# Performance work log

Hardware: AMD Instinct MI355X
Metric: run time of the kernel (lower is better)

## Reference

```python
import jax, jax.numpy as jnp
import numpy as np

B, T, D, H, NL = 64, 1024, 64, 256, 2


def setup_inputs() -> dict:
    key = jax.random.key(0)
    ks = jax.random.split(key, 12)
    s_ih0 = 1.0 / np.sqrt(H)
    inp = {
        "x": jax.random.normal(ks[0], (B, T, D), dtype=jnp.float32),
        "W_ih0": jax.random.uniform(ks[1], (4 * H, D), jnp.float32, -s_ih0, s_ih0),
        "W_hh0": jax.random.uniform(ks[2], (4 * H, H), jnp.float32, -s_ih0, s_ih0),
        "b_ih0": jax.random.uniform(ks[3], (4 * H,), jnp.float32, -s_ih0, s_ih0),
        "b_hh0": jax.random.uniform(ks[4], (4 * H,), jnp.float32, -s_ih0, s_ih0),
        "W_ih1": jax.random.uniform(ks[5], (4 * H, H), jnp.float32, -s_ih0, s_ih0),
        "W_hh1": jax.random.uniform(ks[6], (4 * H, H), jnp.float32, -s_ih0, s_ih0),
        "b_ih1": jax.random.uniform(ks[7], (4 * H,), jnp.float32, -s_ih0, s_ih0),
        "b_hh1": jax.random.uniform(ks[8], (4 * H,), jnp.float32, -s_ih0, s_ih0),
        "fc_w": jax.random.uniform(ks[9], (1, H), jnp.float32, -s_ih0, s_ih0),
        "fc_b": jax.random.uniform(ks[10], (1,), jnp.float32, -s_ih0, s_ih0),
    }
    return inp


def _lstm_layer(x, W_ih, W_hh, b_ih, b_hh):
    # x: [B, T, Din] -> hidden sequence [B, T, H]
    h = W_hh.shape[1]
    # precompute input contribution for all timesteps (PyTorch gate order i,f,g,o)
    xg = jnp.einsum('btd,gd->btg', x, W_ih) + b_ih + b_hh  # [B, T, 4H]

    def step(carry, xt):
        hprev, cprev = carry
        gates = xt + hprev @ W_hh.T  # [B, 4H]
        i, f, g, o = jnp.split(gates, 4, axis=-1)
        i = jax.nn.sigmoid(i)
        f = jax.nn.sigmoid(f)
        g = jnp.tanh(g)
        o = jax.nn.sigmoid(o)
        c = f * cprev + i * g
        hnew = o * jnp.tanh(c)
        return (hnew, c), hnew

    b = x.shape[0]
    h0 = jnp.zeros((b, h), x.dtype)
    _, hs = jax.lax.scan(step, (h0, h0), jnp.swapaxes(xg, 0, 1))
    return jnp.swapaxes(hs, 0, 1)  # [B, T, H]


def reference(x, W_ih0, W_hh0, b_ih0, b_hh0, W_ih1, W_hh1, b_ih1, b_hh1, fc_w, fc_b):
    h1 = _lstm_layer(x, W_ih0, W_hh0, b_ih0, b_hh0)
    h2 = _lstm_layer(h1, W_ih1, W_hh1, b_ih1, b_hh1)
    last = h2[:, -1, :]  # [B, H]
    return last @ fc_w.T + fc_b  # [B, 1]
```

## Files before the change

kernel.cpp:

```cpp
#include <hip/hip_runtime.h>

#define B_ 64
#define TT 1024
#define HH 256

__device__ __forceinline__ float sigmoidf_(float x) { return 1.f / (1.f + __expf(-x)); }
__device__ __forceinline__ float fast_tanh(float x) {
    float e = __expf(2.f * x);
    return 1.f - 2.f / (e + 1.f);
}

__global__ __launch_bounds__(256) void xgemm_kernel(
    const float* __restrict__ A, const float* __restrict__ W,
    const float* __restrict__ bih, const float* __restrict__ bhh,
    float* __restrict__ out,
    int K, int RINGA, int s0A, int LC, int astr)
{
    __shared__ float As[16][132];
    __shared__ float Bs[16][132];
    const int tid = threadIdx.x;
    const int bm = (int)blockIdx.x >> 3;
    const int bn = (int)blockIdx.x & 7;
    const int m0 = bm << 7, n0 = bn << 7;
    const int ty = tid >> 4, tx = tid & 15;
    const int CM = (1 << LC) - 1;

    const float* arow[8];
    const float* brow[8];
#pragma unroll
    for (int i = 0; i < 8; ++i) {
        int mm = m0 + i * 16 + ty;
        int bb = mm >> LC, tc = mm & CM;
        int slot = s0A + tc; if (slot >= RINGA) slot -= RINGA;
        arow[i] = A + ((size_t)bb * RINGA + slot) * K * astr + tx * astr;
        brow[i] = W + (size_t)(n0 + i * 16 + ty) * K + tx;
    }

    float acc[8][8];
#pragma unroll
    for (int i = 0; i < 8; ++i)
#pragma unroll
        for (int j = 0; j < 8; ++j) acc[i][j] = 0.f;

    for (int kc = 0; kc < K; kc += 16) {
#pragma unroll
        for (int i = 0; i < 8; ++i) {
            As[tx][i * 16 + ty] = arow[i][kc * astr];
            Bs[tx][i * 16 + ty] = brow[i][kc];
        }
        __syncthreads();
#pragma unroll
        for (int k = 0; k < 16; ++k) {
            float a[8], bf[8];
#pragma unroll
            for (int j = 0; j < 8; ++j) a[j] = As[k][ty * 8 + j];
#pragma unroll
            for (int j = 0; j < 8; ++j) bf[j] = Bs[k][tx * 8 + j];
#pragma unroll
            for (int i = 0; i < 8; ++i)
#pragma unroll
                for (int j = 0; j < 8; ++j) acc[i][j] = fmaf(a[i], bf[j], acc[i][j]);
        }
        __syncthreads();
    }

    float bias[8];
#pragma unroll
    for (int j = 0; j < 8; ++j) bias[j] = bih[n0 + tx * 8 + j] + bhh[n0 + tx * 8 + j];
#pragma unroll
    for (int i = 0; i < 8; ++i) {
        float4 v0 = make_float4(acc[i][0] + bias[0], acc[i][1] + bias[1],
                                acc[i][2] + bias[2], acc[i][3] + bias[3]);
        float4 v1 = make_float4(acc[i][4] + bias[4], acc[i][5] + bias[5],
                                acc[i][6] + bias[6], acc[i][7] + bias[7]);
        size_t o = (size_t)(m0 + ty * 8 + i) * 1024 + n0 + tx * 8;
        *(float4*)&out[o] = v0;
        *(float4*)&out[o + 4] = v1;
    }
}

__global__ __launch_bounds__(512, 2) void recur_chunk(
    const float* __restrict__ xg,
    const float* __restrict__ Whh,
    unsigned long long* __restrict__ hring,
    float* __restrict__ cstate,
    int t0, int nsteps, int s0, int RING, int LC, int first)
{
    const int tid = threadIdx.x;
    const int b = (int)blockIdx.x & 63;
    const int q = (int)blockIdx.x >> 6;
    const int w = tid >> 6;
    const int l = tid & 63;
    const int hf = l >> 5;
    const int r = w * 32 + (l & 31);
    const int gr = ((r >> 6) << 8) + (q << 6) + (r & 63);

    __shared__ __align__(16) float sh_h[256];
    __shared__ float sh_gate[256];

    float4 w4[32];
    {
        const float4* src = (const float4*)(Whh + (size_t)gr * 256 + (hf << 7));
#pragma unroll
        for (int j = 0; j < 32; ++j) w4[j] = src[j];
    }

    const size_t hbB = (size_t)b * RING;
    float c = 0.f;
    if (!first && tid < 64) c = cstate[((int)blockIdx.x << 6) + tid];
    if (tid < 256) {
        if (first) {
            sh_h[tid] = 0.f;
        } else {
            int sprev = (s0 == 0) ? RING - 1 : s0 - 1;
            unsigned long long v = hring[(hbB + sprev) * 256 + tid];
            sh_h[tid] = __uint_as_float((unsigned)v);
        }
    }
    __syncthreads();

    for (int tc = 0; tc < nsteps; ++tc) {
        const int t = t0 + tc;
        int slot = s0 + tc; if (slot >= RING) slot -= RING;
        const size_t srow = (hbB + slot) * 256;

        float xgv = 0.f;
        if (hf == 0) xgv = xg[((size_t)((b << LC) + tc) << 10) + gr];

        float acc = 0.f;
        const float4* h4 = ((const float4*)sh_h) + (hf << 5);
#pragma unroll
        for (int j = 0; j < 32; ++j) {
            float4 hv = h4[j], wv = w4[j];
            acc = fmaf(wv.x, hv.x, acc);
            acc = fmaf(wv.y, hv.y, acc);
            acc = fmaf(wv.z, hv.z, acc);
            acc = fmaf(wv.w, hv.w, acc);
        }
        acc += __shfl_xor(acc, 32);
        if (hf == 0) sh_gate[r] = acc + xgv;
        __syncthreads();

        if (tid < 64) {
            float gi = sh_gate[tid];
            float gf = sh_gate[64 + tid];
            float gg = sh_gate[128 + tid];
            float go = sh_gate[192 + tid];
            float i_ = sigmoidf_(gi);
            float f_ = sigmoidf_(gf);
            float g_ = fast_tanh(gg);
            float o_ = sigmoidf_(go);
            c = fmaf(f_, c, i_ * g_);
            float hn = o_ * fast_tanh(c);
            sh_h[(q << 6) + tid] = hn;
            unsigned long long word =
                ((unsigned long long)(unsigned)t << 32) | __float_as_uint(hn);
            __hip_atomic_store(&hring[srow + (q << 6) + tid], word,
                               __ATOMIC_RELAXED, __HIP_MEMORY_SCOPE_AGENT);
        } else if (w <= 3) {
            const int p = (q + w) & 3;
            unsigned long long* src = &hring[srow + (p << 6) + l];
            unsigned long long v;
            for (;;) {
                v = __hip_atomic_load(src, __ATOMIC_RELAXED,
                                      __HIP_MEMORY_SCOPE_AGENT);
                if ((int)(v >> 32) == t) break;
                __builtin_amdgcn_s_sleep(1);
            }
            sh_h[(p << 6) + l] = __uint_as_float((unsigned)v);
        }
        __syncthreads();
    }

    if (tid < 64) cstate[((int)blockIdx.x << 6) + tid] = c;
}

__global__ void fc_kernel(const unsigned long long* __restrict__ h2r,
                          int slot_last, int RING,
                          const float* __restrict__ fcw, const float* __restrict__ fcb,
                          float* __restrict__ out)
{
    int b = threadIdx.x;
    if (b < 64) {
        const unsigned long long* h = h2r + ((size_t)b * RING + slot_last) * 256;
        float acc = 0.f;
        for (int d = 0; d < HH; ++d)
            acc = fmaf(__uint_as_float((unsigned)h[d]), fcw[d], acc);
        out[b] = acc + fcb[0];
    }
}

extern "C" void kernel_launch(void* const* d_in, const int* in_sizes, int n_in,
                              void* d_out, int out_size, void* d_ws, size_t ws_size,
                              hipStream_t stream)
{
    const float* x     = (const float*)d_in[0];
    const float* W_ih0 = (const float*)d_in[1];
    const float* W_hh0 = (const float*)d_in[2];
    const float* b_ih0 = (const float*)d_in[3];
    const float* b_hh0 = (const float*)d_in[4];
    const float* W_ih1 = (const float*)d_in[5];
    const float* W_hh1 = (const float*)d_in[6];
    const float* b_ih1 = (const float*)d_in[7];
    const float* b_hh1 = (const float*)d_in[8];
    const float* fc_w  = (const float*)d_in[9];
    const float* fc_b  = (const float*)d_in[10];
    float* out = (float*)d_out;

    auto need = [](size_t CH) -> size_t {
        return 4ull * (65536ull * CH
                     + 65536ull * (CH + 1)
                     + 32768ull);
    };
    int CHUNK = 32, LC = 5;
    if      (ws_size >= need(256)) { CHUNK = 256; LC = 8; }
    else if (ws_size >= need(128)) { CHUNK = 128; LC = 7; }
    else if (ws_size >= need(64))  { CHUNK = 64;  LC = 6; }
    const int RING = CHUNK + 1;

    float* ws  = (float*)d_ws;
    float* xgc = ws;
    unsigned long long* h1r =
        (unsigned long long*)(xgc + 65536ull * CHUNK);
    unsigned long long* h2r = h1r + 16384ull * RING;
    float* c0 = (float*)(h2r + 16384ull * RING);
    float* c1 = c0 + 16384;

    const int nchunks = TT / CHUNK;
    const int gemmblk = (B_ * CHUNK / 128) * 8;

    for (int k = 0; k < nchunks; ++k) {
        const int t0 = k * CHUNK;
        const int s0 = t0 % RING;
        const int first = (k == 0) ? 1 : 0;

        xgemm_kernel<<<dim3(gemmblk), dim3(256), 0, stream>>>(
            x, W_ih0, b_ih0, b_hh0, xgc, 64, TT, t0, LC, 1);
        recur_chunk<<<dim3(256), dim3(512), 0, stream>>>(
            xgc, W_hh0, h1r, c0, t0, CHUNK, s0, RING, LC, first);

        xgemm_kernel<<<dim3(gemmblk), dim3(256), 0, stream>>>(
            (const float*)h1r, W_ih1, b_ih1, b_hh1, xgc, 256, RING, s0, LC, 2);
        recur_chunk<<<dim3(256), dim3(512), 0, stream>>>(
            xgc, W_hh1, h2r, c1, t0, CHUNK, s0, RING, LC, first);
    }

    const int slot_last = (TT - 1) % RING;
    fc_kernel<<<dim3(1), dim3(64), 0, stream>>>(h2r, slot_last, RING, fc_w, fc_b, out);
}
```

Measured before the change: 3.575 ms.

## Split recurrent dot product across four lanes with 1024-thread blocks

The recurrent kernel now uses 1024 threads per block, each handling a quarter of a gate row's 256-element dot product. This halves the per-thread weight registers (16 float4) and reduces results with two lane shuffles. The shared h buffer is padded to 68 floats per quarter to avoid LDS bank conflicts between the four lane groups. The aim is shorter per-step latency on the serial recurrence, at the cost of more waves per block, an extra shuffle and larger barriers.

```diff
diff --git a/kernel.cpp b/kernel.cpp
--- a/kernel.cpp
+++ b/kernel.cpp
@@ -79,7 +79,9 @@
     }
 }
 
-__global__ __launch_bounds__(512, 2) void recur_chunk(
+__global__ __launch_bounds__(1024)
+__attribute__((amdgpu_waves_per_eu(4, 4)))
+void recur_chunk(
     const float* __restrict__ xg,
     const float* __restrict__ Whh,
     unsigned long long* __restrict__ hring,
@@ -91,33 +93,35 @@
     const int q = (int)blockIdx.x >> 6;
     const int w = tid >> 6;
     const int l = tid & 63;
-    const int hf = l >> 5;
-    const int r = w * 32 + (l & 31);
+    const int r = tid >> 2;
+    const int c4 = tid & 3;
     const int gr = ((r >> 6) << 8) + (q << 6) + (r & 63);
 
-    __shared__ __align__(16) float sh_h[256];
+    __shared__ __align__(16) float sh_h[272];
     __shared__ float sh_gate[256];
 
-    float4 w4[32];
+    float4 w4[16];
     {
-        const float4* src = (const float4*)(Whh + (size_t)gr * 256 + (hf << 7));
-#pragma unroll
-        for (int j = 0; j < 32; ++j) w4[j] = src[j];
-    }
+        const float4* src = (const float4*)(Whh + (size_t)gr * 256 + (c4 << 6));
+#pragma unroll
+        for (int j = 0; j < 16; ++j) w4[j] = src[j];
+    }
+#pragma unroll
+    for (int j = 0; j < 16; ++j)
+        asm volatile("" : "+v"(w4[j].x), "+v"(w4[j].y), "+v"(w4[j].z), "+v"(w4[j].w));
 
     const size_t hbB = (size_t)b * RING;
     float c = 0.f;
     if (!first && tid < 64) c = cstate[((int)blockIdx.x << 6) + tid];
-    if (tid < 256) {
-        if (first) {
-            sh_h[tid] = 0.f;
-        } else {
-            int sprev = (s0 == 0) ? RING - 1 : s0 - 1;
-            unsigned long long v = hring[(hbB + sprev) * 256 + tid];
-            sh_h[tid] = __uint_as_float((unsigned)v);
-        }
+    if (tid < 272) sh_h[tid] = 0.f;
+    if (!first && tid < 256) {
+        int sprev = (s0 == 0) ? RING - 1 : s0 - 1;
+        unsigned long long v = hring[(hbB + sprev) * 256 + tid];
+        sh_h[tid + ((tid >> 6) << 2)] = __uint_as_float((unsigned)v);
     }
     __syncthreads();
+
+    const float4* h4 = (const float4*)(sh_h + c4 * 68);
 
     for (int tc = 0; tc < nsteps; ++tc) {
         const int t = t0 + tc;
@@ -125,37 +129,37 @@
         const size_t srow = (hbB + slot) * 256;
 
         float xgv = 0.f;
-        if (hf == 0) xgv = xg[((size_t)((b << LC) + tc) << 10) + gr];
+        if (c4 == 0) xgv = xg[((size_t)((b << LC) + tc) << 10) + gr];
 
         float acc = 0.f;
-        const float4* h4 = ((const float4*)sh_h) + (hf << 5);
-#pragma unroll
-        for (int j = 0; j < 32; ++j) {
+#pragma unroll
+        for (int j = 0; j < 16; ++j) {
             float4 hv = h4[j], wv = w4[j];
             acc = fmaf(wv.x, hv.x, acc);
             acc = fmaf(wv.y, hv.y, acc);
             acc = fmaf(wv.z, hv.z, acc);
             acc = fmaf(wv.w, hv.w, acc);
         }
-        acc += __shfl_xor(acc, 32);
-        if (hf == 0) sh_gate[r] = acc + xgv;
-        __syncthreads();
-
-        if (tid < 64) {
-            float gi = sh_gate[tid];
-            float gf = sh_gate[64 + tid];
-            float gg = sh_gate[128 + tid];
-            float go = sh_gate[192 + tid];
+        acc += __shfl_xor(acc, 1);
+        acc += __shfl_xor(acc, 2);
+        if (c4 == 0) sh_gate[r] = acc + xgv;
+        __syncthreads();
+
+        if (w == 0) {
+            float gi = sh_gate[l];
+            float gf = sh_gate[64 + l];
+            float gg = sh_gate[128 + l];
+            float go = sh_gate[192 + l];
             float i_ = sigmoidf_(gi);
             float f_ = sigmoidf_(gf);
             float g_ = fast_tanh(gg);
             float o_ = sigmoidf_(go);
             c = fmaf(f_, c, i_ * g_);
             float hn = o_ * fast_tanh(c);
-            sh_h[(q << 6) + tid] = hn;
+            sh_h[q * 68 + l] = hn;
             unsigned long long word =
                 ((unsigned long long)(unsigned)t << 32) | __float_as_uint(hn);
-            __hip_atomic_store(&hring[srow + (q << 6) + tid], word,
+            __hip_atomic_store(&hring[srow + (q << 6) + l], word,
                                __ATOMIC_RELAXED, __HIP_MEMORY_SCOPE_AGENT);
         } else if (w <= 3) {
             const int p = (q + w) & 3;
@@ -167,7 +171,7 @@
                 if ((int)(v >> 32) == t) break;
                 __builtin_amdgcn_s_sleep(1);
             }
-            sh_h[(p << 6) + l] = __uint_as_float((unsigned)v);
+            sh_h[p * 68 + l] = __uint_as_float((unsigned)v);
         }
         __syncthreads();
     }
@@ -236,12 +240,12 @@
 
         xgemm_kernel<<<dim3(gemmblk), dim3(256), 0, stream>>>(
             x, W_ih0, b_ih0, b_hh0, xgc, 64, TT, t0, LC, 1);
-        recur_chunk<<<dim3(256), dim3(512), 0, stream>>>(
+        recur_chunk<<<dim3(256), dim3(1024), 0, stream>>>(
             xgc, W_hh0, h1r, c0, t0, CHUNK, s0, RING, LC, first);
 
         xgemm_kernel<<<dim3(gemmblk), dim3(256), 0, stream>>>(
             (const float*)h1r, W_ih1, b_ih1, b_hh1, xgc, 256, RING, s0, LC, 2);
-        recur_chunk<<<dim3(256), dim3(512), 0, stream>>>(
+        recur_chunk<<<dim3(256), dim3(1024), 0, stream>>>(
             xgc, W_hh1, h2r, c1, t0, CHUNK, s0, RING, LC, first);
     }
 
```

Measured after the change: 3.572 ms. No clear change (-0.1%).

## Remap recurrent gate rows per wave to drop a barrier and double-buffer h

Applied to the files above, without the earlier changes.

Reassigns gate rows so that each wave holds the i, f, g and o rows for 8 hidden units. The four gates can then be gathered with wave shuffles instead of going through a shared gate buffer, which removes one __syncthreads per timestep. The hidden state in shared memory becomes double-buffered and padded to avoid bank conflicts. The next step's xg value is prefetched, the dot product is split across four accumulators, and the cell update runs at raised wave priority. The cost is that more lanes sit idle during the cell update, since only 8 lanes per wave compute it, and the indexing becomes more involved.

```diff
diff --git a/kernel.cpp b/kernel.cpp
--- a/kernel.cpp
+++ b/kernel.cpp
@@ -79,7 +79,9 @@
     }
 }
 
-__global__ __launch_bounds__(512, 2) void recur_chunk(
+__global__ __launch_bounds__(512)
+__attribute__((amdgpu_waves_per_eu(2, 2)))
+void recur_chunk(
     const float* __restrict__ xg,
     const float* __restrict__ Whh,
     unsigned long long* __restrict__ hring,
@@ -92,11 +94,12 @@
     const int w = tid >> 6;
     const int l = tid & 63;
     const int hf = l >> 5;
-    const int r = w * 32 + (l & 31);
-    const int gr = ((r >> 6) << 8) + (q << 6) + (r & 63);
-
-    __shared__ __align__(16) float sh_h[256];
-    __shared__ float sh_gate[256];
+    const int g = (l & 31) >> 3;
+    const int k = l & 7;
+    const int d = (w << 3) + k;
+    const int gr = (g << 8) + (q << 6) + d;
+
+    __shared__ __align__(16) float sh_h[2][272];
 
     float4 w4[32];
     {
@@ -107,57 +110,70 @@
 
     const size_t hbB = (size_t)b * RING;
     float c = 0.f;
-    if (!first && tid < 64) c = cstate[((int)blockIdx.x << 6) + tid];
-    if (tid < 256) {
-        if (first) {
-            sh_h[tid] = 0.f;
-        } else {
-            int sprev = (s0 == 0) ? RING - 1 : s0 - 1;
-            unsigned long long v = hring[(hbB + sprev) * 256 + tid];
-            sh_h[tid] = __uint_as_float((unsigned)v);
-        }
+    if (!first && l < 8) c = cstate[((int)blockIdx.x << 6) + d];
+    if (tid < 272) { sh_h[0][tid] = 0.f; sh_h[1][tid] = 0.f; }
+    if (!first && tid < 256) {
+        int sprev = (s0 == 0) ? RING - 1 : s0 - 1;
+        unsigned long long v = hring[(hbB + sprev) * 256 + tid];
+        sh_h[(t0 + 1) & 1][tid + ((tid >> 6) << 2)] = __uint_as_float((unsigned)v);
     }
     __syncthreads();
+
+    const float* xgp = xg + ((size_t)(b << LC) << 10) + gr;
+    float xgv = (hf == 0) ? xgp[0] : 0.f;
 
     for (int tc = 0; tc < nsteps; ++tc) {
         const int t = t0 + tc;
         int slot = s0 + tc; if (slot >= RING) slot -= RING;
         const size_t srow = (hbB + slot) * 256;
 
-        float xgv = 0.f;
-        if (hf == 0) xgv = xg[((size_t)((b << LC) + tc) << 10) + gr];
-
-        float acc = 0.f;
-        const float4* h4 = ((const float4*)sh_h) + (hf << 5);
-#pragma unroll
-        for (int j = 0; j < 32; ++j) {
-            float4 hv = h4[j], wv = w4[j];
-            acc = fmaf(wv.x, hv.x, acc);
-            acc = fmaf(wv.y, hv.y, acc);
-            acc = fmaf(wv.z, hv.z, acc);
-            acc = fmaf(wv.w, hv.w, acc);
-        }
+        float xgn = 0.f;
+        if (hf == 0 && tc + 1 < nsteps) xgn = xgp[(size_t)(tc + 1) << 10];
+
+        const float* shr = sh_h[(t + 1) & 1];
+        float* shw = sh_h[t & 1];
+
+        const float4* h4a = (const float4*)(shr + hf * 136);
+        const float4* h4b = (const float4*)(shr + hf * 136 + 68);
+        float a0 = 0.f, a1 = 0.f, a2 = 0.f, a3 = 0.f;
+#pragma unroll
+        for (int j = 0; j < 16; ++j) {
+            float4 hv = h4a[j], wv = w4[j];
+            a0 = fmaf(wv.x, hv.x, a0); a1 = fmaf(wv.y, hv.y, a1);
+            a2 = fmaf(wv.z, hv.z, a2); a3 = fmaf(wv.w, hv.w, a3);
+        }
+#pragma unroll
+        for (int j = 0; j < 16; ++j) {
+            float4 hv = h4b[j], wv = w4[16 + j];
+            a0 = fmaf(wv.x, hv.x, a0); a1 = fmaf(wv.y, hv.y, a1);
+            a2 = fmaf(wv.z, hv.z, a2); a3 = fmaf(wv.w, hv.w, a3);
+        }
+        float acc = (a0 + a1) + (a2 + a3);
         acc += __shfl_xor(acc, 32);
-        if (hf == 0) sh_gate[r] = acc + xgv;
-        __syncthreads();
-
-        if (tid < 64) {
-            float gi = sh_gate[tid];
-            float gf = sh_gate[64 + tid];
-            float gg = sh_gate[128 + tid];
-            float go = sh_gate[192 + tid];
-            float i_ = sigmoidf_(gi);
-            float f_ = sigmoidf_(gf);
-            float g_ = fast_tanh(gg);
-            float o_ = sigmoidf_(go);
+        float gv = acc + xgv;
+        xgv = xgn;
+
+        float fv = __shfl(gv, 8 + k);
+        float gG = __shfl(gv, 16 + k);
+        float ov = __shfl(gv, 24 + k);
+
+        __builtin_amdgcn_s_setprio(1);
+        if (l < 8) {
+            float i_ = sigmoidf_(gv);
+            float f_ = sigmoidf_(fv);
+            float g_ = fast_tanh(gG);
+            float o_ = sigmoidf_(ov);
             c = fmaf(f_, c, i_ * g_);
             float hn = o_ * fast_tanh(c);
-            sh_h[(q << 6) + tid] = hn;
+            shw[q * 68 + d] = hn;
             unsigned long long word =
                 ((unsigned long long)(unsigned)t << 32) | __float_as_uint(hn);
-            __hip_atomic_store(&hring[srow + (q << 6) + tid], word,
+            __hip_atomic_store(&hring[srow + (q << 6) + d], word,
                                __ATOMIC_RELAXED, __HIP_MEMORY_SCOPE_AGENT);
-        } else if (w <= 3) {
+        }
+        __builtin_amdgcn_s_setprio(0);
+
+        if (w >= 1 && w <= 3) {
             const int p = (q + w) & 3;
             unsigned long long* src = &hring[srow + (p << 6) + l];
             unsigned long long v;
@@ -167,12 +183,12 @@
                 if ((int)(v >> 32) == t) break;
                 __builtin_amdgcn_s_sleep(1);
             }
-            sh_h[(p << 6) + l] = __uint_as_float((unsigned)v);
+            shw[p * 68 + l] = __uint_as_float((unsigned)v);
         }
         __syncthreads();
     }
 
-    if (tid < 64) cstate[((int)blockIdx.x << 6) + tid] = c;
+    if (l < 8) cstate[((int)blockIdx.x << 6) + d] = c;
 }
 
 __global__ void fc_kernel(const unsigned long long* __restrict__ h2r,
```

After: 4.764 ms. 33.3% more time.
